# Optimization experiments

Measured on AMD Instinct MI355X. Metric: run time of the kernel, lower is better.

## Reference

```python
import jax, jax.numpy as jnp
from jax import lax
import numpy as np

C_IN, C_OUT, G, K, PAD = 64, 128, 4, 3, 1
P = K * K
CG = C_IN // G
N, H, W = 8, 64, 64
LN_EPS = 1e-6
BN_EPS = 1e-5


def setup_inputs() -> dict:
    key = jax.random.key(0)
    ks = jax.random.split(key, 32)
    r = lambda i, shape, s=0.05: jax.random.normal(ks[i], shape, dtype=jnp.float32) * s
    return dict(
        x=jax.random.normal(ks[0], (N, C_IN, H, W), dtype=jnp.float32),
        reflectance=jax.random.uniform(ks[1], (N, 1, H, W), dtype=jnp.float32),
        gain_w1=r(2, (C_IN, C_IN // 4)), gain_b1=r(3, (C_IN // 4,)),
        gain_w2=r(4, (C_IN // 4, C_IN)), gain_b2=r(5, (C_IN,)),
        tap_w=r(6, (C_IN,)), tap_b=r(7, (C_IN,)),
        dw_w=r(8, (K, K, 1, C_IN)), dw_b=r(9, (C_IN,)),
        ln_g=jnp.ones((C_IN,), jnp.float32), ln_b=jnp.zeros((C_IN,), jnp.float32),
        inp_w=r(10, (C_IN, C_IN)), inp_b=r(11, (C_IN,)),
        off_w=r(12, (C_IN, G * P * 2), 0.02), off_b=r(13, (G * P * 2,), 0.02),
        mask_w=r(14, (C_IN, G * P), 0.02), mask_b=r(15, (G * P,), 0.02),
        outp_w=r(16, (C_IN, C_IN)), outp_b=r(17, (C_IN,)),
        conv_w=r(18, (C_IN, C_OUT)), conv_b=r(19, (C_OUT,)),
        bn1_g=jnp.ones((C_IN,), jnp.float32), bn1_b=jnp.zeros((C_IN,), jnp.float32),
        bn1_m=r(20, (C_IN,)),
        bn1_v=jax.random.uniform(ks[21], (C_IN,), minval=0.5, maxval=1.5),
        bn2_g=jnp.ones((C_OUT,), jnp.float32), bn2_b=jnp.zeros((C_OUT,), jnp.float32),
        bn2_m=r(22, (C_OUT,)),
        bn2_v=jax.random.uniform(ks[23], (C_OUT,), minval=0.5, maxval=1.5),
    )


def _bilinear_gather(xg, py, px):
    # xg: (N, Hp, Wp, G, CG); py/px: (N, H, W, G, P) absolute pixel coords
    # replicates F.grid_sample(mode='bilinear', padding_mode='zeros', align_corners=False)
    n_, Hp, Wp = xg.shape[0], xg.shape[1], xg.shape[2]
    y0 = jnp.floor(py)
    x0 = jnp.floor(px)
    wy = py - y0
    wx = px - x0
    nI = jnp.arange(n_).reshape(n_, 1, 1, 1, 1)
    gI = jnp.arange(G).reshape(1, 1, 1, G, 1)
    out = jnp.zeros(py.shape + (CG,), xg.dtype)
    for dy in (0, 1):
        for dx in (0, 1):
            yi = y0 + dy
            xi = x0 + dx
            w = (wy if dy else 1.0 - wy) * (wx if dx else 1.0 - wx)
            valid = (yi >= 0) & (yi < Hp) & (xi >= 0) & (xi < Wp)
            yc = jnp.clip(yi, 0, Hp - 1).astype(jnp.int32)
            xc = jnp.clip(xi, 0, Wp - 1).astype(jnp.int32)
            v = xg[nI, yc, xc, gI]  # (N, H, W, G, P, CG)
            out = out + (w * valid.astype(w.dtype))[..., None] * v
    return out


def reference(x, reflectance, gain_w1, gain_b1, gain_w2, gain_b2, tap_w, tap_b,
              dw_w, dw_b, ln_g, ln_b, inp_w, inp_b, off_w, off_b, mask_w, mask_b,
              outp_w, outp_b, conv_w, conv_b, bn1_g, bn1_b, bn1_m, bn1_v,
              bn2_g, bn2_b, bn2_m, bn2_v):
    n_, c_, h_, w_ = x.shape
    # ---- GainBlock (SE-style): x * sigmoid(mlp(avgpool(x))) + x ----
    pooled = x.mean(axis=(2, 3))                               # (N, C)
    g = jax.nn.relu(pooled @ gain_w1 + gain_b1)
    gain = jax.nn.sigmoid(g @ gain_w2 + gain_b2)               # (N, C)
    x = x * gain[:, :, None, None] + x
    # ---- ReflectiveFeedback: x + relu(conv1x1(reflectance)) ----
    refl = jax.nn.relu(reflectance * tap_w[None, :, None, None] + tap_b[None, :, None, None])
    x = x + refl                                               # (N, C, H, W)
    # ---- DCNv3 (pytorch version, group=4, k=3, pad=1, stride=1) ----
    xh = jnp.transpose(x, (0, 2, 3, 1))                        # NHWC
    xp = xh @ inp_w + inp_b                                    # input_proj
    dw = lax.conv_general_dilated(xh, dw_w, (1, 1), 'SAME',
                                  feature_group_count=c_,
                                  dimension_numbers=('NHWC', 'HWIO', 'NHWC')) + dw_b
    mu = dw.mean(-1, keepdims=True)
    var = dw.var(-1, keepdims=True)
    dw = ln_g * (dw - mu) * lax.rsqrt(var + LN_EPS) + ln_b     # LN channels_last
    dw = jax.nn.gelu(dw, approximate=False)
    offset = (dw @ off_w + off_b).reshape(n_, h_, w_, G, P, 2)
    mask = jax.nn.softmax((dw @ mask_w + mask_b).reshape(n_, h_, w_, G, P), axis=-1)
    # dcnv3_core: pad input, build reference + dilation grids (normalized by padded size)
    xpad = jnp.pad(xp, ((0, 0), (PAD, PAD), (PAD, PAD), (0, 0)))
    Hp, Wp = h_ + 2 * PAD, w_ + 2 * PAD
    ctr = (K - 1) // 2  # = (dilation*(k-1))//2 with dilation=1
    ref_y = (jnp.arange(h_, dtype=jnp.float32) + ctr + 0.5) / Hp
    ref_x = (jnp.arange(w_, dtype=jnp.float32) + ctr + 0.5) / Wp
    kk = jnp.arange(K, dtype=jnp.float32) - ctr                # [-1, 0, 1]
    gx = jnp.repeat(kk, K) / Wp                                # w-outer, h-inner order
    gy = jnp.tile(kk, K) / Hp
    loc_x = (ref_x[None, None, :, None, None] + gx[None, None, None, None, :]
             + offset[..., 0] / Wp)                            # (N,H,W,G,P)
    loc_y = (ref_y[None, :, None, None, None] + gy[None, None, None, None, :]
             + offset[..., 1] / Hp)
    px = loc_x * Wp - 0.5   # align_corners=False pixel coords
    py = loc_y * Hp - 0.5
    xg = xpad.reshape(n_, Hp, Wp, G, CG)
    samp = _bilinear_gather(xg, py, px)                        # (N,H,W,G,P,CG)
    dcn = (samp * mask[..., None]).sum(axis=4).reshape(n_, h_, w_, c_)
    dcn = dcn @ outp_w + outp_b                                # output_proj
    y = jnp.transpose(dcn, (0, 3, 1, 2))                       # back to NCHW
    # ---- bn1 -> relu -> conv1x1 -> bn2 -> relu (eval-mode BN) ----
    y = bn1_g[None, :, None, None] * (y - bn1_m[None, :, None, None]) \
        * lax.rsqrt(bn1_v[None, :, None, None] + BN_EPS) + bn1_b[None, :, None, None]
    y = jax.nn.relu(y)
    y = jnp.einsum('nchw,cd->ndhw', y, conv_w) + conv_b[None, :, None, None]
    y = bn2_g[None, :, None, None] * (y - bn2_m[None, :, None, None]) \
        * lax.rsqrt(bn2_v[None, :, None, None] + BN_EPS) + bn2_b[None, :, None, None]
    return jax.nn.relu(y)
```

## Files before the change

kernel.cpp:

```cpp
#include <hip/hip_runtime.h>
#include <math.h>


#define WAVE_FENCE() asm volatile("s_waitcnt lgkmcnt(0)" ::: "memory")

__device__ __forceinline__ float2 fma2s(float s, float2 v, float2 acc) {
    acc.x = fmaf(s, v.x, acc.x);
    acc.y = fmaf(s, v.y, acc.y);
    return acc;
}

__global__ __launch_bounds__(256) void k_pool(const float* x, float* pooled) {
    __shared__ float red[256];
    int b = blockIdx.x;
    int nc = ((b & 7) << 6) | (b >> 3);
    const float4* p4 = reinterpret_cast<const float4*>(x + (size_t)nc * 4096);
    float s = 0.f;
    for (int i = threadIdx.x; i < 1024; i += 256) {
        float4 v = p4[i];
        s += v.x + v.y + v.z + v.w;
    }
    red[threadIdx.x] = s;
    __syncthreads();
    for (int o = 128; o > 0; o >>= 1) {
        if (threadIdx.x < o) red[threadIdx.x] += red[threadIdx.x + o];
        __syncthreads();
    }
    if (threadIdx.x == 0) pooled[nc] = red[0] * (1.f / 4096.f);
}

__global__ __launch_bounds__(256) void k_xsproj(
        const float* x, const float* refl,
        const float* tap_w, const float* tap_b,
        const float* pooled,
        const float* gw1, const float* gb1,
        const float* gw2, const float* gb2,
        const float* inp_w, const float* inp_b,
        float* xs, float* xpad) {
    __shared__ float tile[64][65];
    __shared__ float xsw[64][68];
    __shared__ float rr[64];
    __shared__ float gbuf[64];
    int t = threadIdx.x;
    int b = blockIdx.x;
    int n = b & 7, h = b >> 3;
    int c = t & 63, g = t >> 6;

    #pragma unroll
    for (int it = 0; it < 4; ++it) {
        int f = it * 256 + t;
        int cc = f >> 4, w4 = (f & 15) * 4;
        float4 v = *reinterpret_cast<const float4*>(
            &x[(((size_t)(n * 64 + cc)) * 64 + h) * 64 + w4]);
        tile[cc][w4 + 0] = v.x;
        tile[cc][w4 + 1] = v.y;
        tile[cc][w4 + 2] = v.z;
        tile[cc][w4 + 3] = v.w;
    }
    if (t < 64) rr[t] = refl[n * 4096 + h * 64 + t];
    if (t >= 64 && t < 128) {
        int lane = t - 64;
        float pv = pooled[n * 64 + lane];
        float part[16];
        const float4* g4 = reinterpret_cast<const float4*>(gw1 + lane * 16);
        #pragma unroll
        for (int q = 0; q < 4; ++q) {
            float4 v = g4[q];
            part[q * 4 + 0] = pv * v.x;
            part[q * 4 + 1] = pv * v.y;
            part[q * 4 + 2] = pv * v.z;
            part[q * 4 + 3] = pv * v.w;
        }
        #pragma unroll
        for (int o = 32; o > 0; o >>= 1) {
            #pragma unroll
            for (int j = 0; j < 16; ++j) part[j] += __shfl_xor(part[j], o, 64);
        }
        float acc = gb2[lane];
        #pragma unroll
        for (int j = 0; j < 16; ++j) {
            float hj = fmaxf(part[j] + gb1[j], 0.f);
            acc += hj * gw2[j * 64 + lane];
        }
        gbuf[lane] = 1.f + 1.f / (1.f + __expf(-acc));
    }
    __syncthreads();

    {
        float gv = gbuf[c];
        float tw = tap_w[c], tb = tap_b[c];
        float* xsg = xs + (((size_t)(n * 64 + h)) * 64) * 64 + c;
        #pragma unroll
        for (int k = 0; k < 16; ++k) {
            int w = g * 16 + k;
            float r = fmaxf(rr[w] * tw + tb, 0.f);
            float v = tile[c][w] * gv + r;
            xsw[w][c] = v;
            xsg[(size_t)w * 64] = v;
        }
    }
    __syncthreads();

    {
        float acc[16];
        float bv = inp_b[c];
        #pragma unroll
        for (int k = 0; k < 16; ++k) acc[k] = bv;
        for (int c4 = 0; c4 < 64; c4 += 4) {
            float q0 = inp_w[(c4 + 0) * 64 + c];
            float q1 = inp_w[(c4 + 1) * 64 + c];
            float q2 = inp_w[(c4 + 2) * 64 + c];
            float q3 = inp_w[(c4 + 3) * 64 + c];
            #pragma unroll
            for (int k = 0; k < 16; ++k) {
                float4 d = *reinterpret_cast<const float4*>(&xsw[g * 16 + k][c4]);
                acc[k] += d.x * q0 + d.y * q1 + d.z * q2 + d.w * q3;
            }
        }
        const size_t rowb = (((size_t)n * 66) + (h + 1)) * 66;
        #pragma unroll
        for (int k = 0; k < 16; ++k) {
            int w = g * 16 + k;
            xpad[(rowb + (w + 1)) * 64 + c] = acc[k];
        }
        if (g == 0) xpad[rowb * 64 + c] = 0.f;
        if (g == 3) xpad[(rowb + 65) * 64 + c] = 0.f;
        if (h == 0 || h == 63) {
            const size_t base = ((((size_t)n * 66) + (h == 0 ? 0 : 65)) * 66) * 64;
            for (int i = t; i < 66 * 64; i += 256) xpad[base + i] = 0.f;
        }
    }
}

__global__ __launch_bounds__(128, 4) void k_dwsamp(const float* xs, const float* xpad,
                       const float* dw_w, const float* dw_b,
                       const float* ln_g, const float* ln_b,
                       const float* off_w, const float* off_b,
                       const float* mask_w, const float* mask_b,
                       const float* outp_w, const float* outp_b,
                       const float* bn1_g, const float* bn1_b,
                       const float* bn1_m, const float* bn1_v,
                       const float* conv_w, const float* conv_b,
                       const float* bn2_g, const float* bn2_b,
                       const float* bn2_m, const float* bn2_v,
                       float* out) {
    __shared__ float smem[2816];

    int tid = threadIdx.x;
    int lane = tid & 63, wv = tid >> 6;
    float*  chunk = smem + wv * 1408;
    int4*   sad   = reinterpret_cast<int4*>(chunk);
    float*  dwr   = chunk;
    float4* swt   = reinterpret_cast<float4*>(chunk + 576);
    float*  dcnl  = chunk + 1152;
    float*  mlog  = chunk + 1152;

    int b = blockIdx.x;
    int n = b & 7;
    int pos0 = (b >> 3) * 8 + wv * 4;
    int h = pos0 >> 6, w0 = pos0 & 63;

    {
        float dwk[9];
        #pragma unroll
        for (int k = 0; k < 9; ++k) dwk[k] = dw_w[k * 64 + lane];
        float s[4];
        float bvv = dw_b[lane];
        #pragma unroll
        for (int p = 0; p < 4; ++p) s[p] = bvv;
        for (int ky = 0; ky < 3; ++ky) {
            int y = h + ky - 1;
            if (y < 0 || y > 63) continue;
            const float* xrow = xs + ((size_t)(n * 64 + y)) * 4096;
            float v[6];
            #pragma unroll
            for (int dx = 0; dx < 6; ++dx) {
                int x2 = w0 - 1 + dx;
                v[dx] = (x2 >= 0 && x2 <= 63) ? xrow[x2 * 64 + lane] : 0.f;
            }
            float k0 = dwk[ky * 3 + 0], k1 = dwk[ky * 3 + 1], k2 = dwk[ky * 3 + 2];
            #pragma unroll
            for (int p = 0; p < 4; ++p)
                s[p] += v[p] * k0 + v[p + 1] * k1 + v[p + 2] * k2;
        }
        float lngv = ln_g[lane], lnbv = ln_b[lane];
        #pragma unroll
        for (int p = 0; p < 4; ++p) {
            float sv = s[p];
            float sum = sv, sq = sv * sv;
            #pragma unroll
            for (int o = 32; o > 0; o >>= 1) {
                sum += __shfl_xor(sum, o, 64);
                sq  += __shfl_xor(sq,  o, 64);
            }
            float mu = sum * (1.f / 64.f);
            float var = sq * (1.f / 64.f) - mu * mu;
            float nrm = (sv - mu) * rsqrtf(var + 1e-6f) * lngv + lnbv;
            dwr[p * 64 + lane] = 0.5f * nrm * (1.f + erff(nrm * 0.70710678118654752f));
        }
    }
    WAVE_FENCE();

    float2 a01[4];
    {
        int jb = lane * 2;
        const float* wptr;
        int stride;
        float b0 = 0.f, b1 = 0.f;
        if (lane < 36)      { wptr = off_w + jb;         stride = 72; b0 = off_b[jb];       b1 = off_b[jb + 1]; }
        else if (lane < 54) { wptr = mask_w + (jb - 72); stride = 36; b0 = mask_b[jb - 72]; b1 = mask_b[jb - 71]; }
        else                { wptr = off_w;              stride = 0; }
        #pragma unroll
        for (int p = 0; p < 4; ++p) a01[p] = make_float2(b0, b1);
        for (int c4 = 0; c4 < 64; c4 += 4) {
            float4 d0 = *reinterpret_cast<const float4*>(&dwr[0 * 64 + c4]);
            float4 d1 = *reinterpret_cast<const float4*>(&dwr[1 * 64 + c4]);
            float4 d2 = *reinterpret_cast<const float4*>(&dwr[2 * 64 + c4]);
            float4 d3 = *reinterpret_cast<const float4*>(&dwr[3 * 64 + c4]);
            float dk0[4] = {d0.x, d0.y, d0.z, d0.w};
            float dk1[4] = {d1.x, d1.y, d1.z, d1.w};
            float dk2[4] = {d2.x, d2.y, d2.z, d2.w};
            float dk3[4] = {d3.x, d3.y, d3.z, d3.w};
            #pragma unroll
            for (int k = 0; k < 4; ++k) {
                float2 w2 = *reinterpret_cast<const float2*>(wptr);
                wptr += stride;
                a01[0] = fma2s(dk0[k], w2, a01[0]);
                a01[1] = fma2s(dk1[k], w2, a01[1]);
                a01[2] = fma2s(dk2[k], w2, a01[2]);
                a01[3] = fma2s(dk3[k], w2, a01[3]);
            }
        }
        if (lane >= 36 && lane < 54) {
            int jm = lane * 2 - 72;
            #pragma unroll
            for (int p = 0; p < 4; ++p) {
                mlog[p * 40 + jm]     = a01[p].x;
                mlog[p * 40 + jm + 1] = a01[p].y;
            }
        }
    }
    WAVE_FENCE();

    if (lane < 36) {
        int g = lane / 9, pp = lane - g * 9;
        #pragma unroll
        for (int p = 0; p < 4; ++p) {
            const float* lrow = &mlog[p * 40 + g * 9];
            float m = lrow[0];
            #pragma unroll
            for (int k = 1; k < 9; ++k) m = fmaxf(m, lrow[k]);
            float ssum = 0.f, ek = 0.f;
            #pragma unroll
            for (int k = 0; k < 9; ++k) {
                float e = __expf(lrow[k] - m);
                ssum += e;
                if (k == pp) ek = e;
            }
            float mk = ek / ssum;
            float px = (float)((w0 + p) + (pp / 3)) + a01[p].x;
            float py = (float)(h + (pp % 3)) + a01[p].y;
            float x0f = floorf(px), y0f = floorf(py);
            float wx = px - x0f, wy = py - y0f;
            int x0 = (int)x0f, y0 = (int)y0f;
            int x1 = x0 + 1, y1 = y0 + 1;
            int xc0 = min(max(x0, 0), 65), xc1 = min(max(x1, 0), 65);
            int yc0 = min(max(y0, 0), 65), yc1 = min(max(y1, 0), 65);
            float vx0 = (x0 >= 0 && x0 < 66) ? 1.f : 0.f;
            float vx1 = (x1 >= 0 && x1 < 66) ? 1.f : 0.f;
            float vy0 = (y0 >= 0 && y0 < 66) ? 1.f : 0.f;
            float vy1 = (y1 >= 0 && y1 < 66) ? 1.f : 0.f;
            float wx0 = (1.f - wx) * vx0, wx1 = wx * vx1;
            float wy0 = (1.f - wy) * vy0, wy1 = wy * vy1;
            swt[p * 36 + lane] = make_float4(mk * wy0 * wx0, mk * wy0 * wx1,
                                             mk * wy1 * wx0, mk * wy1 * wx1);
            sad[p * 36 + lane] = make_int4((yc0 * 66 + xc0) * 64, (yc0 * 66 + xc1) * 64,
                                           (yc1 * 66 + xc0) * 64, (yc1 * 66 + xc1) * 64);
        }
    }
    WAVE_FENCE();

    {
        int gb = (lane >> 4) * 9;
        const float* xpn = xpad + (size_t)n * 66 * 66 * 64;
        #pragma unroll
        for (int p = 0; p < 4; ++p) {
            float t0[9], t1[9], t2[9], t3[9];
            #pragma unroll
            for (int pp = 0; pp < 9; ++pp) {
                int4 a = sad[p * 36 + gb + pp];
                t0[pp] = xpn[a.x + lane];
                t1[pp] = xpn[a.y + lane];
                t2[pp] = xpn[a.z + lane];
                t3[pp] = xpn[a.w + lane];
            }
            float acc = 0.f;
            #pragma unroll
            for (int pp = 0; pp < 9; ++pp) {
                float4 cw = swt[p * 36 + gb + pp];
                acc += cw.x * t0[pp] + cw.y * t1[pp]
                     + cw.z * t2[pp] + cw.w * t3[pp];
            }
            dcnl[p * 64 + lane] = acc;
        }
    }
    WAVE_FENCE();

    {
        float ob = outp_b[lane];
        float2 s01 = make_float2(ob, ob), s23 = make_float2(ob, ob);
        for (int c4 = 0; c4 < 64; c4 += 4) {
            float w0v = outp_w[(c4 + 0) * 64 + lane];
            float w1v = outp_w[(c4 + 1) * 64 + lane];
            float w2v = outp_w[(c4 + 2) * 64 + lane];
            float w3v = outp_w[(c4 + 3) * 64 + lane];
            float4 d0 = *reinterpret_cast<const float4*>(&dcnl[0 * 64 + c4]);
            float4 d1 = *reinterpret_cast<const float4*>(&dcnl[1 * 64 + c4]);
            float4 d2 = *reinterpret_cast<const float4*>(&dcnl[2 * 64 + c4]);
            float4 d3 = *reinterpret_cast<const float4*>(&dcnl[3 * 64 + c4]);
            s01 = fma2s(w0v, make_float2(d0.x, d1.x), s01);
            s01 = fma2s(w1v, make_float2(d0.y, d1.y), s01);
            s01 = fma2s(w2v, make_float2(d0.z, d1.z), s01);
            s01 = fma2s(w3v, make_float2(d0.w, d1.w), s01);
            s23 = fma2s(w0v, make_float2(d2.x, d3.x), s23);
            s23 = fma2s(w1v, make_float2(d2.y, d3.y), s23);
            s23 = fma2s(w2v, make_float2(d2.z, d3.z), s23);
            s23 = fma2s(w3v, make_float2(d2.w, d3.w), s23);
        }
        float sc = bn1_g[lane] * rsqrtf(bn1_v[lane] + 1e-5f);
        float sh = bn1_b[lane] - sc * bn1_m[lane];
        WAVE_FENCE();
        dcnl[0 * 64 + lane] = fmaxf(sc * s01.x + sh, 0.f);
        dcnl[1 * 64 + lane] = fmaxf(sc * s01.y + sh, 0.f);
        dcnl[2 * 64 + lane] = fmaxf(sc * s23.x + sh, 0.f);
        dcnl[3 * 64 + lane] = fmaxf(sc * s23.y + sh, 0.f);
    }
    WAVE_FENCE();

    {
        float2 acc2[4];
        #pragma unroll
        for (int p = 0; p < 4; ++p) acc2[p] = make_float2(0.f, 0.f);
        for (int c4 = 0; c4 < 64; c4 += 4) {
            float4 d0 = *reinterpret_cast<const float4*>(&dcnl[0 * 64 + c4]);
            float4 d1 = *reinterpret_cast<const float4*>(&dcnl[1 * 64 + c4]);
            float4 d2 = *reinterpret_cast<const float4*>(&dcnl[2 * 64 + c4]);
            float4 d3 = *reinterpret_cast<const float4*>(&dcnl[3 * 64 + c4]);
            float dk0[4] = {d0.x, d0.y, d0.z, d0.w};
            float dk1[4] = {d1.x, d1.y, d1.z, d1.w};
            float dk2[4] = {d2.x, d2.y, d2.z, d2.w};
            float dk3[4] = {d3.x, d3.y, d3.z, d3.w};
            #pragma unroll
            for (int k = 0; k < 4; ++k) {
                float2 w2 = make_float2(conv_w[(c4 + k) * 128 + lane],
                                        conv_w[(c4 + k) * 128 + 64 + lane]);
                acc2[0] = fma2s(dk0[k], w2, acc2[0]);
                acc2[1] = fma2s(dk1[k], w2, acc2[1]);
                acc2[2] = fma2s(dk2[k], w2, acc2[2]);
                acc2[3] = fma2s(dk3[k], w2, acc2[3]);
            }
        }
        int dA = lane, dB = lane + 64;
        float scA = bn2_g[dA] * rsqrtf(bn2_v[dA] + 1e-5f);
        float shA = scA * (conv_b[dA] - bn2_m[dA]) + bn2_b[dA];
        float scB = bn2_g[dB] * rsqrtf(bn2_v[dB] + 1e-5f);
        float shB = scB * (conv_b[dB] - bn2_m[dB]) + bn2_b[dB];
        float4 rA, rB;
        rA.x = fmaxf(scA * acc2[0].x + shA, 0.f);
        rA.y = fmaxf(scA * acc2[1].x + shA, 0.f);
        rA.z = fmaxf(scA * acc2[2].x + shA, 0.f);
        rA.w = fmaxf(scA * acc2[3].x + shA, 0.f);
        rB.x = fmaxf(scB * acc2[0].y + shB, 0.f);
        rB.y = fmaxf(scB * acc2[1].y + shB, 0.f);
        rB.z = fmaxf(scB * acc2[2].y + shB, 0.f);
        rB.w = fmaxf(scB * acc2[3].y + shB, 0.f);
        size_t oA = (((size_t)(n * 128 + dA)) * 64 + h) * 64 + w0;
        size_t oB = (((size_t)(n * 128 + dB)) * 64 + h) * 64 + w0;
        *reinterpret_cast<float4*>(out + oA) = rA;
        *reinterpret_cast<float4*>(out + oB) = rB;
    }
}

extern "C" void kernel_launch(void* const* d_in, const int* in_sizes, int n_in,
                              void* d_out, int out_size, void* d_ws, size_t ws_size,
                              hipStream_t stream) {
    const float* x      = (const float*)d_in[0];
    const float* refl   = (const float*)d_in[1];
    const float* gw1    = (const float*)d_in[2];
    const float* gb1    = (const float*)d_in[3];
    const float* gw2    = (const float*)d_in[4];
    const float* gb2    = (const float*)d_in[5];
    const float* tap_w  = (const float*)d_in[6];
    const float* tap_b  = (const float*)d_in[7];
    const float* dw_w   = (const float*)d_in[8];
    const float* dw_b   = (const float*)d_in[9];
    const float* ln_g   = (const float*)d_in[10];
    const float* ln_b   = (const float*)d_in[11];
    const float* inp_w  = (const float*)d_in[12];
    const float* inp_b  = (const float*)d_in[13];
    const float* off_w  = (const float*)d_in[14];
    const float* off_b  = (const float*)d_in[15];
    const float* mask_w = (const float*)d_in[16];
    const float* mask_b = (const float*)d_in[17];
    const float* outp_w = (const float*)d_in[18];
    const float* outp_b = (const float*)d_in[19];
    const float* conv_w = (const float*)d_in[20];
    const float* conv_b = (const float*)d_in[21];
    const float* bn1_g  = (const float*)d_in[22];
    const float* bn1_b  = (const float*)d_in[23];
    const float* bn1_m  = (const float*)d_in[24];
    const float* bn1_v  = (const float*)d_in[25];
    const float* bn2_g  = (const float*)d_in[26];
    const float* bn2_b  = (const float*)d_in[27];
    const float* bn2_m  = (const float*)d_in[28];
    const float* bn2_v  = (const float*)d_in[29];

    float* ws     = (float*)d_ws;
    float* pooled = ws;
    float* xs     = ws + 512;
    float* xpad   = xs + 2097152;

    k_pool<<<512, 256, 0, stream>>>(x, pooled);
    k_xsproj<<<512, 256, 0, stream>>>(x, refl, tap_w, tap_b, pooled,
                                      gw1, gb1, gw2, gb2,
                                      inp_w, inp_b, xs, xpad);
    k_dwsamp<<<4096, 128, 0, stream>>>(xs, xpad, dw_w, dw_b, ln_g, ln_b,
                                       off_w, off_b, mask_w, mask_b,
                                       outp_w, outp_b, bn1_g, bn1_b, bn1_m, bn1_v,
                                       conv_w, conv_b, bn2_g, bn2_b, bn2_m, bn2_v,
                                       (float*)d_out);
}
```

Baseline: 190.5 us.

## Process eight pixels per wave in fused deformable-conv kernel to reuse weights

Each wave now handles eight output pixels instead of four, doubling the per-wave shared memory chunk and halving the grid. Weight loads for the offset/mask projection, output projection and the 1x1 conv are amortized across twice as many pixels, and the depthwise conv reuses overlapping input columns. The cost is higher register pressure and LDS use per block, which can reduce occupancy under the launch bounds, and fewer blocks to fill the GPU.

```diff
diff --git a/kernel.cpp b/kernel.cpp
--- a/kernel.cpp
+++ b/kernel.cpp
@@ -144,48 +144,48 @@
                        const float* bn2_g, const float* bn2_b,
                        const float* bn2_m, const float* bn2_v,
                        float* out) {
-    __shared__ float smem[2816];
+    __shared__ float smem[5632];
 
     int tid = threadIdx.x;
     int lane = tid & 63, wv = tid >> 6;
-    float*  chunk = smem + wv * 1408;
+    float*  chunk = smem + wv * 2816;
     int4*   sad   = reinterpret_cast<int4*>(chunk);
     float*  dwr   = chunk;
-    float4* swt   = reinterpret_cast<float4*>(chunk + 576);
-    float*  dcnl  = chunk + 1152;
-    float*  mlog  = chunk + 1152;
+    float4* swt   = reinterpret_cast<float4*>(chunk + 1152);
+    float*  dcnl  = chunk + 2304;
+    float*  mlog  = chunk + 2304;
 
     int b = blockIdx.x;
     int n = b & 7;
-    int pos0 = (b >> 3) * 8 + wv * 4;
+    int pos0 = (b >> 3) * 16 + wv * 8;
     int h = pos0 >> 6, w0 = pos0 & 63;
 
     {
         float dwk[9];
         #pragma unroll
         for (int k = 0; k < 9; ++k) dwk[k] = dw_w[k * 64 + lane];
-        float s[4];
+        float s[8];
         float bvv = dw_b[lane];
         #pragma unroll
-        for (int p = 0; p < 4; ++p) s[p] = bvv;
+        for (int p = 0; p < 8; ++p) s[p] = bvv;
         for (int ky = 0; ky < 3; ++ky) {
             int y = h + ky - 1;
             if (y < 0 || y > 63) continue;
             const float* xrow = xs + ((size_t)(n * 64 + y)) * 4096;
-            float v[6];
-            #pragma unroll
-            for (int dx = 0; dx < 6; ++dx) {
+            float v[10];
+            #pragma unroll
+            for (int dx = 0; dx < 10; ++dx) {
                 int x2 = w0 - 1 + dx;
                 v[dx] = (x2 >= 0 && x2 <= 63) ? xrow[x2 * 64 + lane] : 0.f;
             }
             float k0 = dwk[ky * 3 + 0], k1 = dwk[ky * 3 + 1], k2 = dwk[ky * 3 + 2];
             #pragma unroll
-            for (int p = 0; p < 4; ++p)
+            for (int p = 0; p < 8; ++p)
                 s[p] += v[p] * k0 + v[p + 1] * k1 + v[p + 2] * k2;
         }
         float lngv = ln_g[lane], lnbv = ln_b[lane];
         #pragma unroll
-        for (int p = 0; p < 4; ++p) {
+        for (int p = 0; p < 8; ++p) {
             float sv = s[p];
             float sum = sv, sq = sv * sv;
             #pragma unroll
@@ -201,7 +201,7 @@
     }
     WAVE_FENCE();
 
-    float2 a01[4];
+    float2 a01[8];
     {
         int jb = lane * 2;
         const float* wptr;
@@ -211,30 +211,37 @@
         else if (lane < 54) { wptr = mask_w + (jb - 72); stride = 36; b0 = mask_b[jb - 72]; b1 = mask_b[jb - 71]; }
         else                { wptr = off_w;              stride = 0; }
         #pragma unroll
-        for (int p = 0; p < 4; ++p) a01[p] = make_float2(b0, b1);
+        for (int p = 0; p < 8; ++p) a01[p] = make_float2(b0, b1);
         for (int c4 = 0; c4 < 64; c4 += 4) {
-            float4 d0 = *reinterpret_cast<const float4*>(&dwr[0 * 64 + c4]);
-            float4 d1 = *reinterpret_cast<const float4*>(&dwr[1 * 64 + c4]);
-            float4 d2 = *reinterpret_cast<const float4*>(&dwr[2 * 64 + c4]);
-            float4 d3 = *reinterpret_cast<const float4*>(&dwr[3 * 64 + c4]);
-            float dk0[4] = {d0.x, d0.y, d0.z, d0.w};
-            float dk1[4] = {d1.x, d1.y, d1.z, d1.w};
-            float dk2[4] = {d2.x, d2.y, d2.z, d2.w};
-            float dk3[4] = {d3.x, d3.y, d3.z, d3.w};
+            float2 w2a[4];
             #pragma unroll
             for (int k = 0; k < 4; ++k) {
-                float2 w2 = *reinterpret_cast<const float2*>(wptr);
+                w2a[k] = *reinterpret_cast<const float2*>(wptr);
                 wptr += stride;
-                a01[0] = fma2s(dk0[k], w2, a01[0]);
-                a01[1] = fma2s(dk1[k], w2, a01[1]);
-                a01[2] = fma2s(dk2[k], w2, a01[2]);
-                a01[3] = fma2s(dk3[k], w2, a01[3]);
+            }
+            #pragma unroll
+            for (int hf = 0; hf < 2; ++hf) {
+                float4 d0 = *reinterpret_cast<const float4*>(&dwr[(hf * 4 + 0) * 64 + c4]);
+                float4 d1 = *reinterpret_cast<const float4*>(&dwr[(hf * 4 + 1) * 64 + c4]);
+                float4 d2 = *reinterpret_cast<const float4*>(&dwr[(hf * 4 + 2) * 64 + c4]);
+                float4 d3 = *reinterpret_cast<const float4*>(&dwr[(hf * 4 + 3) * 64 + c4]);
+                float dk0[4] = {d0.x, d0.y, d0.z, d0.w};
+                float dk1[4] = {d1.x, d1.y, d1.z, d1.w};
+                float dk2[4] = {d2.x, d2.y, d2.z, d2.w};
+                float dk3[4] = {d3.x, d3.y, d3.z, d3.w};
+                #pragma unroll
+                for (int k = 0; k < 4; ++k) {
+                    a01[hf * 4 + 0] = fma2s(dk0[k], w2a[k], a01[hf * 4 + 0]);
+                    a01[hf * 4 + 1] = fma2s(dk1[k], w2a[k], a01[hf * 4 + 1]);
+                    a01[hf * 4 + 2] = fma2s(dk2[k], w2a[k], a01[hf * 4 + 2]);
+                    a01[hf * 4 + 3] = fma2s(dk3[k], w2a[k], a01[hf * 4 + 3]);
+                }
             }
         }
         if (lane >= 36 && lane < 54) {
             int jm = lane * 2 - 72;
             #pragma unroll
-            for (int p = 0; p < 4; ++p) {
+            for (int p = 0; p < 8; ++p) {
                 mlog[p * 40 + jm]     = a01[p].x;
                 mlog[p * 40 + jm + 1] = a01[p].y;
             }
@@ -245,7 +252,7 @@
     if (lane < 36) {
         int g = lane / 9, pp = lane - g * 9;
         #pragma unroll
-        for (int p = 0; p < 4; ++p) {
+        for (int p = 0; p < 8; ++p) {
             const float* lrow = &mlog[p * 40 + g * 9];
             float m = lrow[0];
             #pragma unroll
@@ -284,7 +291,7 @@
         int gb = (lane >> 4) * 9;
         const float* xpn = xpad + (size_t)n * 66 * 66 * 64;
         #pragma unroll
-        for (int p = 0; p < 4; ++p) {
+        for (int p = 0; p < 8; ++p) {
             float t0[9], t1[9], t2[9], t3[9];
             #pragma unroll
             for (int pp = 0; pp < 9; ++pp) {
@@ -308,56 +315,62 @@
 
     {
         float ob = outp_b[lane];
-        float2 s01 = make_float2(ob, ob), s23 = make_float2(ob, ob);
+        float2 sp[4];
+        #pragma unroll
+        for (int q = 0; q < 4; ++q) sp[q] = make_float2(ob, ob);
         for (int c4 = 0; c4 < 64; c4 += 4) {
             float w0v = outp_w[(c4 + 0) * 64 + lane];
             float w1v = outp_w[(c4 + 1) * 64 + lane];
             float w2v = outp_w[(c4 + 2) * 64 + lane];
             float w3v = outp_w[(c4 + 3) * 64 + lane];
-            float4 d0 = *reinterpret_cast<const float4*>(&dcnl[0 * 64 + c4]);
-            float4 d1 = *reinterpret_cast<const float4*>(&dcnl[1 * 64 + c4]);
-            float4 d2 = *reinterpret_cast<const float4*>(&dcnl[2 * 64 + c4]);
-            float4 d3 = *reinterpret_cast<const float4*>(&dcnl[3 * 64 + c4]);
-            s01 = fma2s(w0v, make_float2(d0.x, d1.x), s01);
-            s01 = fma2s(w1v, make_float2(d0.y, d1.y), s01);
-            s01 = fma2s(w2v, make_float2(d0.z, d1.z), s01);
-            s01 = fma2s(w3v, make_float2(d0.w, d1.w), s01);
-            s23 = fma2s(w0v, make_float2(d2.x, d3.x), s23);
-            s23 = fma2s(w1v, make_float2(d2.y, d3.y), s23);
-            s23 = fma2s(w2v, make_float2(d2.z, d3.z), s23);
-            s23 = fma2s(w3v, make_float2(d2.w, d3.w), s23);
+            #pragma unroll
+            for (int q = 0; q < 4; ++q) {
+                float4 da = *reinterpret_cast<const float4*>(&dcnl[(2 * q + 0) * 64 + c4]);
+                float4 db = *reinterpret_cast<const float4*>(&dcnl[(2 * q + 1) * 64 + c4]);
+                sp[q] = fma2s(w0v, make_float2(da.x, db.x), sp[q]);
+                sp[q] = fma2s(w1v, make_float2(da.y, db.y), sp[q]);
+                sp[q] = fma2s(w2v, make_float2(da.z, db.z), sp[q]);
+                sp[q] = fma2s(w3v, make_float2(da.w, db.w), sp[q]);
+            }
         }
         float sc = bn1_g[lane] * rsqrtf(bn1_v[lane] + 1e-5f);
         float sh = bn1_b[lane] - sc * bn1_m[lane];
         WAVE_FENCE();
-        dcnl[0 * 64 + lane] = fmaxf(sc * s01.x + sh, 0.f);
-        dcnl[1 * 64 + lane] = fmaxf(sc * s01.y + sh, 0.f);
-        dcnl[2 * 64 + lane] = fmaxf(sc * s23.x + sh, 0.f);
-        dcnl[3 * 64 + lane] = fmaxf(sc * s23.y + sh, 0.f);
+        #pragma unroll
+        for (int q = 0; q < 4; ++q) {
+            dcnl[(2 * q + 0) * 64 + lane] = fmaxf(sc * sp[q].x + sh, 0.f);
+            dcnl[(2 * q + 1) * 64 + lane] = fmaxf(sc * sp[q].y + sh, 0.f);
+        }
     }
     WAVE_FENCE();
 
     {
-        float2 acc2[4];
-        #pragma unroll
-        for (int p = 0; p < 4; ++p) acc2[p] = make_float2(0.f, 0.f);
+        float2 acc2[8];
+        #pragma unroll
+        for (int p = 0; p < 8; ++p) acc2[p] = make_float2(0.f, 0.f);
         for (int c4 = 0; c4 < 64; c4 += 4) {
-            float4 d0 = *reinterpret_cast<const float4*>(&dcnl[0 * 64 + c4]);
-            float4 d1 = *reinterpret_cast<const float4*>(&dcnl[1 * 64 + c4]);
-            float4 d2 = *reinterpret_cast<const float4*>(&dcnl[2 * 64 + c4]);
-            float4 d3 = *reinterpret_cast<const float4*>(&dcnl[3 * 64 + c4]);
-            float dk0[4] = {d0.x, d0.y, d0.z, d0.w};
-            float dk1[4] = {d1.x, d1.y, d1.z, d1.w};
-            float dk2[4] = {d2.x, d2.y, d2.z, d2.w};
-            float dk3[4] = {d3.x, d3.y, d3.z, d3.w};
-            #pragma unroll
-            for (int k = 0; k < 4; ++k) {
-                float2 w2 = make_float2(conv_w[(c4 + k) * 128 + lane],
-                                        conv_w[(c4 + k) * 128 + 64 + lane]);
-                acc2[0] = fma2s(dk0[k], w2, acc2[0]);
-                acc2[1] = fma2s(dk1[k], w2, acc2[1]);
-                acc2[2] = fma2s(dk2[k], w2, acc2[2]);
-                acc2[3] = fma2s(dk3[k], w2, acc2[3]);
+            float2 w2a[4];
+            #pragma unroll
+            for (int k = 0; k < 4; ++k)
+                w2a[k] = make_float2(conv_w[(c4 + k) * 128 + lane],
+                                     conv_w[(c4 + k) * 128 + 64 + lane]);
+            #pragma unroll
+            for (int hf = 0; hf < 2; ++hf) {
+                float4 d0 = *reinterpret_cast<const float4*>(&dcnl[(hf * 4 + 0) * 64 + c4]);
+                float4 d1 = *reinterpret_cast<const float4*>(&dcnl[(hf * 4 + 1) * 64 + c4]);
+                float4 d2 = *reinterpret_cast<const float4*>(&dcnl[(hf * 4 + 2) * 64 + c4]);
+                float4 d3 = *reinterpret_cast<const float4*>(&dcnl[(hf * 4 + 3) * 64 + c4]);
+                float dk0[4] = {d0.x, d0.y, d0.z, d0.w};
+                float dk1[4] = {d1.x, d1.y, d1.z, d1.w};
+                float dk2[4] = {d2.x, d2.y, d2.z, d2.w};
+                float dk3[4] = {d3.x, d3.y, d3.z, d3.w};
+                #pragma unroll
+                for (int k = 0; k < 4; ++k) {
+                    acc2[hf * 4 + 0] = fma2s(dk0[k], w2a[k], acc2[hf * 4 + 0]);
+                    acc2[hf * 4 + 1] = fma2s(dk1[k], w2a[k], acc2[hf * 4 + 1]);
+                    acc2[hf * 4 + 2] = fma2s(dk2[k], w2a[k], acc2[hf * 4 + 2]);
+                    acc2[hf * 4 + 3] = fma2s(dk3[k], w2a[k], acc2[hf * 4 + 3]);
+                }
             }
         }
         int dA = lane, dB = lane + 64;
@@ -365,19 +378,22 @@
         float shA = scA * (conv_b[dA] - bn2_m[dA]) + bn2_b[dA];
         float scB = bn2_g[dB] * rsqrtf(bn2_v[dB] + 1e-5f);
         float shB = scB * (conv_b[dB] - bn2_m[dB]) + bn2_b[dB];
-        float4 rA, rB;
-        rA.x = fmaxf(scA * acc2[0].x + shA, 0.f);
-        rA.y = fmaxf(scA * acc2[1].x + shA, 0.f);
-        rA.z = fmaxf(scA * acc2[2].x + shA, 0.f);
-        rA.w = fmaxf(scA * acc2[3].x + shA, 0.f);
-        rB.x = fmaxf(scB * acc2[0].y + shB, 0.f);
-        rB.y = fmaxf(scB * acc2[1].y + shB, 0.f);
-        rB.z = fmaxf(scB * acc2[2].y + shB, 0.f);
-        rB.w = fmaxf(scB * acc2[3].y + shB, 0.f);
         size_t oA = (((size_t)(n * 128 + dA)) * 64 + h) * 64 + w0;
         size_t oB = (((size_t)(n * 128 + dB)) * 64 + h) * 64 + w0;
-        *reinterpret_cast<float4*>(out + oA) = rA;
-        *reinterpret_cast<float4*>(out + oB) = rB;
+        #pragma unroll
+        for (int hf = 0; hf < 2; ++hf) {
+            float4 rA, rB;
+            rA.x = fmaxf(scA * acc2[hf * 4 + 0].x + shA, 0.f);
+            rA.y = fmaxf(scA * acc2[hf * 4 + 1].x + shA, 0.f);
+            rA.z = fmaxf(scA * acc2[hf * 4 + 2].x + shA, 0.f);
+            rA.w = fmaxf(scA * acc2[hf * 4 + 3].x + shA, 0.f);
+            rB.x = fmaxf(scB * acc2[hf * 4 + 0].y + shB, 0.f);
+            rB.y = fmaxf(scB * acc2[hf * 4 + 1].y + shB, 0.f);
+            rB.z = fmaxf(scB * acc2[hf * 4 + 2].y + shB, 0.f);
+            rB.w = fmaxf(scB * acc2[hf * 4 + 3].y + shB, 0.f);
+            *reinterpret_cast<float4*>(out + oA + hf * 4) = rA;
+            *reinterpret_cast<float4*>(out + oB + hf * 4) = rB;
+        }
     }
 }
 
@@ -424,7 +440,7 @@
     k_xsproj<<<512, 256, 0, stream>>>(x, refl, tap_w, tap_b, pooled,
                                       gw1, gb1, gw2, gb2,
                                       inp_w, inp_b, xs, xpad);
-    k_dwsamp<<<4096, 128, 0, stream>>>(xs, xpad, dw_w, dw_b, ln_g, ln_b,
+    k_dwsamp<<<2048, 128, 0, stream>>>(xs, xpad, dw_w, dw_b, ln_g, ln_b,
                                        off_w, off_b, mask_w, mask_b,
                                        outp_w, outp_b, bn1_g, bn1_b, bn1_m, bn1_v,
                                        conv_w, conv_b, bn2_g, bn2_b, bn2_m, bn2_v,
```

New measurement: 205.6 us. 8.0% more time.

## Fuse global pooling into projection kernel via per-batch atomic grid sync

Applied to the files above, without the earlier changes.

Removes the separate pooling kernel, which read all of x a second time. Each block of the projection kernel now writes per-row channel partial sums, and the last block to finish for each batch (found with an atomic counter) computes the gain MLP and sets a flag. All blocks of that batch spin on the flag before applying the gain. This saves one full pass over x and one launch, but it adds a memset and relies on every block of a batch being resident at once, which risks deadlock or stalls if they are not.

```diff
diff --git a/kernel.cpp b/kernel.cpp
--- a/kernel.cpp
+++ b/kernel.cpp
@@ -10,41 +10,24 @@
     return acc;
 }
 
-__global__ __launch_bounds__(256) void k_pool(const float* x, float* pooled) {
-    __shared__ float red[256];
-    int b = blockIdx.x;
-    int nc = ((b & 7) << 6) | (b >> 3);
-    const float4* p4 = reinterpret_cast<const float4*>(x + (size_t)nc * 4096);
-    float s = 0.f;
-    for (int i = threadIdx.x; i < 1024; i += 256) {
-        float4 v = p4[i];
-        s += v.x + v.y + v.z + v.w;
-    }
-    red[threadIdx.x] = s;
-    __syncthreads();
-    for (int o = 128; o > 0; o >>= 1) {
-        if (threadIdx.x < o) red[threadIdx.x] += red[threadIdx.x + o];
-        __syncthreads();
-    }
-    if (threadIdx.x == 0) pooled[nc] = red[0] * (1.f / 4096.f);
-}
-
-__global__ __launch_bounds__(256) void k_xsproj(
+__global__ __launch_bounds__(256) void k_pre(
         const float* x, const float* refl,
         const float* tap_w, const float* tap_b,
-        const float* pooled,
         const float* gw1, const float* gb1,
         const float* gw2, const float* gb2,
         const float* inp_w, const float* inp_b,
+        int* sync, float* gaing, float* parts,
         float* xs, float* xpad) {
     __shared__ float tile[64][65];
     __shared__ float xsw[64][68];
     __shared__ float rr[64];
-    __shared__ float gbuf[64];
+    __shared__ int comp;
     int t = threadIdx.x;
     int b = blockIdx.x;
     int n = b & 7, h = b >> 3;
     int c = t & 63, g = t >> 6;
+    int* cnt  = sync;
+    int* flag = sync + 8;
 
     #pragma unroll
     for (int it = 0; it < 4; ++it) {
@@ -58,36 +41,76 @@
         tile[cc][w4 + 3] = v.w;
     }
     if (t < 64) rr[t] = refl[n * 4096 + h * 64 + t];
-    if (t >= 64 && t < 128) {
-        int lane = t - 64;
-        float pv = pooled[n * 64 + lane];
-        float part[16];
-        const float4* g4 = reinterpret_cast<const float4*>(gw1 + lane * 16);
-        #pragma unroll
-        for (int q = 0; q < 4; ++q) {
-            float4 v = g4[q];
-            part[q * 4 + 0] = pv * v.x;
-            part[q * 4 + 1] = pv * v.y;
-            part[q * 4 + 2] = pv * v.z;
-            part[q * 4 + 3] = pv * v.w;
-        }
-        #pragma unroll
-        for (int o = 32; o > 0; o >>= 1) {
-            #pragma unroll
-            for (int j = 0; j < 16; ++j) part[j] += __shfl_xor(part[j], o, 64);
-        }
-        float acc = gb2[lane];
-        #pragma unroll
-        for (int j = 0; j < 16; ++j) {
-            float hj = fmaxf(part[j] + gb1[j], 0.f);
-            acc += hj * gw2[j * 64 + lane];
-        }
-        gbuf[lane] = 1.f + 1.f / (1.f + __expf(-acc));
-    }
-    __syncthreads();
-
-    {
-        float gv = gbuf[c];
+    __syncthreads();
+
+    {
+        float rs = 0.f;
+        #pragma unroll
+        for (int k = 0; k < 16; ++k) rs += tile[c][g * 16 + k];
+        xsw[g][c] = rs;
+    }
+    __syncthreads();
+    if (t < 64) {
+        float tot = xsw[0][t] + xsw[1][t] + xsw[2][t] + xsw[3][t];
+        parts[((size_t)(n * 64 + h)) * 64 + t] = tot;
+    }
+    __syncthreads();
+    if (t == 0) {
+        __threadfence();
+        int old = __hip_atomic_fetch_add(&cnt[n], 1, __ATOMIC_ACQ_REL,
+                                         __HIP_MEMORY_SCOPE_AGENT);
+        comp = (old == 63) ? 1 : 0;
+    }
+    __syncthreads();
+
+    if (comp) {
+        if (t < 64) {
+            __builtin_amdgcn_fence(__ATOMIC_ACQUIRE, "agent");
+            int lane = t;
+            float pv = 0.f;
+            for (int hh = 0; hh < 64; ++hh)
+                pv += parts[((size_t)(n * 64 + hh)) * 64 + lane];
+            pv *= (1.f / 4096.f);
+            float part[16];
+            const float4* g4 = reinterpret_cast<const float4*>(gw1 + lane * 16);
+            #pragma unroll
+            for (int q = 0; q < 4; ++q) {
+                float4 v = g4[q];
+                part[q * 4 + 0] = pv * v.x;
+                part[q * 4 + 1] = pv * v.y;
+                part[q * 4 + 2] = pv * v.z;
+                part[q * 4 + 3] = pv * v.w;
+            }
+            #pragma unroll
+            for (int o = 32; o > 0; o >>= 1) {
+                #pragma unroll
+                for (int j = 0; j < 16; ++j) part[j] += __shfl_xor(part[j], o, 64);
+            }
+            float acc = gb2[lane];
+            #pragma unroll
+            for (int j = 0; j < 16; ++j) {
+                float hj = fmaxf(part[j] + gb1[j], 0.f);
+                acc += hj * gw2[j * 64 + lane];
+            }
+            gaing[n * 64 + lane] = 1.f + 1.f / (1.f + __expf(-acc));
+        }
+        __syncthreads();
+        if (t == 0) {
+            __threadfence();
+            __hip_atomic_store(&flag[n], 1, __ATOMIC_RELEASE,
+                               __HIP_MEMORY_SCOPE_AGENT);
+        }
+    }
+    if (t == 0) {
+        while (__hip_atomic_load(&flag[n], __ATOMIC_RELAXED,
+                                 __HIP_MEMORY_SCOPE_AGENT) == 0)
+            __builtin_amdgcn_s_sleep(16);
+        __builtin_amdgcn_fence(__ATOMIC_ACQUIRE, "agent");
+    }
+    __syncthreads();
+
+    {
+        float gv = gaing[n * 64 + c];
         float tw = tap_w[c], tb = tap_b[c];
         float* xsg = xs + (((size_t)(n * 64 + h)) * 64) * 64 + c;
         #pragma unroll
@@ -416,14 +439,16 @@
     const float* bn2_v  = (const float*)d_in[29];
 
     float* ws     = (float*)d_ws;
-    float* pooled = ws;
-    float* xs     = ws + 512;
+    int*   sync   = (int*)ws;
+    float* gaing  = ws + 16;
+    float* parts  = ws + 528;
+    float* xs     = ws + 33296;
     float* xpad   = xs + 2097152;
 
-    k_pool<<<512, 256, 0, stream>>>(x, pooled);
-    k_xsproj<<<512, 256, 0, stream>>>(x, refl, tap_w, tap_b, pooled,
-                                      gw1, gb1, gw2, gb2,
-                                      inp_w, inp_b, xs, xpad);
+    hipMemsetAsync(sync, 0, 16 * sizeof(int), stream);
+    k_pre<<<512, 256, 0, stream>>>(x, refl, tap_w, tap_b,
+                                   gw1, gb1, gw2, gb2, inp_w, inp_b,
+                                   sync, gaing, parts, xs, xpad);
     k_dwsamp<<<4096, 128, 0, stream>>>(xs, xpad, dw_w, dw_b, ln_g, ln_b,
                                        off_w, off_b, mask_w, mask_b,
                                        outp_w, outp_b, bn1_g, bn1_b, bn1_m, bn1_v,
```

New measurement: 212.1 us. +11.3%, slower.

## Store padded features as horizontal pixel pairs for float2 bilinear gathers

Applied to the files above, without the earlier changes.

The producer kernel now writes each padded pixel's channels interleaved with its right neighbour's (pair layout, 128 floats per position). The sampler can then fetch both horizontal bilinear corners with one float2 load, halving the gather instructions and the address table in shared memory. Edge handling remaps the x weights onto the left and right slots of the clamped base. This doubles the xpad workspace and the write traffic in the producer, and it relies on the workspace being large enough.

```diff
diff --git a/kernel.cpp b/kernel.cpp
--- a/kernel.cpp
+++ b/kernel.cpp
@@ -7,6 +7,11 @@
 __device__ __forceinline__ float2 fma2s(float s, float2 v, float2 acc) {
     acc.x = fmaf(s, v.x, acc.x);
     acc.y = fmaf(s, v.y, acc.y);
+    return acc;
+}
+__device__ __forceinline__ float2 fma22(float2 a, float2 v, float2 acc) {
+    acc.x = fmaf(a.x, v.x, acc.x);
+    acc.y = fmaf(a.y, v.y, acc.y);
     return acc;
 }
 
@@ -36,7 +41,7 @@
         const float* gw1, const float* gb1,
         const float* gw2, const float* gb2,
         const float* inp_w, const float* inp_b,
-        float* xs, float* xpad) {
+        float* xs, float* xpad2) {
     __shared__ float tile[64][65];
     __shared__ float xsw[64][68];
     __shared__ float rr[64];
@@ -120,19 +125,21 @@
         const size_t rowb = (((size_t)n * 66) + (h + 1)) * 66;
         #pragma unroll
         for (int k = 0; k < 16; ++k) {
-            int w = g * 16 + k;
-            xpad[(rowb + (w + 1)) * 64 + c] = acc[k];
-        }
-        if (g == 0) xpad[rowb * 64 + c] = 0.f;
-        if (g == 3) xpad[(rowb + 65) * 64 + c] = 0.f;
+            int xx = g * 16 + k + 1;
+            float v = acc[k];
+            xpad2[(rowb + xx) * 128 + c * 2 + 0]     = v;
+            xpad2[(rowb + xx - 1) * 128 + c * 2 + 1] = v;
+        }
+        if (g == 0) xpad2[rowb * 128 + c * 2 + 0] = 0.f;
+        if (g == 3) xpad2[(rowb + 64) * 128 + c * 2 + 1] = 0.f;
         if (h == 0 || h == 63) {
-            const size_t base = ((((size_t)n * 66) + (h == 0 ? 0 : 65)) * 66) * 64;
-            for (int i = t; i < 66 * 64; i += 256) xpad[base + i] = 0.f;
-        }
-    }
-}
-
-__global__ __launch_bounds__(128, 4) void k_dwsamp(const float* xs, const float* xpad,
+            const size_t base = ((((size_t)n * 66) + (h == 0 ? 0 : 65)) * 66) * 128;
+            for (int i = t; i < 66 * 128; i += 256) xpad2[base + i] = 0.f;
+        }
+    }
+}
+
+__global__ __launch_bounds__(128, 4) void k_dwsamp(const float* xs, const float* xpad2,
                        const float* dw_w, const float* dw_b,
                        const float* ln_g, const float* ln_b,
                        const float* off_w, const float* off_b,
@@ -144,16 +151,16 @@
                        const float* bn2_g, const float* bn2_b,
                        const float* bn2_m, const float* bn2_v,
                        float* out) {
-    __shared__ float smem[2816];
+    __shared__ float smem[2240];
 
     int tid = threadIdx.x;
     int lane = tid & 63, wv = tid >> 6;
-    float*  chunk = smem + wv * 1408;
-    int4*   sad   = reinterpret_cast<int4*>(chunk);
+    float*  chunk = smem + wv * 1120;
+    int2*   sad2  = reinterpret_cast<int2*>(chunk);
     float*  dwr   = chunk;
-    float4* swt   = reinterpret_cast<float4*>(chunk + 576);
-    float*  dcnl  = chunk + 1152;
-    float*  mlog  = chunk + 1152;
+    float4* swt   = reinterpret_cast<float4*>(chunk + 288);
+    float*  dcnl  = chunk + 864;
+    float*  mlog  = chunk + 864;
 
     int b = blockIdx.x;
     int n = b & 7;
@@ -264,44 +271,45 @@
             float wx = px - x0f, wy = py - y0f;
             int x0 = (int)x0f, y0 = (int)y0f;
             int x1 = x0 + 1, y1 = y0 + 1;
-            int xc0 = min(max(x0, 0), 65), xc1 = min(max(x1, 0), 65);
             int yc0 = min(max(y0, 0), 65), yc1 = min(max(y1, 0), 65);
-            float vx0 = (x0 >= 0 && x0 < 66) ? 1.f : 0.f;
-            float vx1 = (x1 >= 0 && x1 < 66) ? 1.f : 0.f;
             float vy0 = (y0 >= 0 && y0 < 66) ? 1.f : 0.f;
             float vy1 = (y1 >= 0 && y1 < 66) ? 1.f : 0.f;
-            float wx0 = (1.f - wx) * vx0, wx1 = wx * vx1;
-            float wy0 = (1.f - wy) * vy0, wy1 = wy * vy1;
-            swt[p * 36 + lane] = make_float4(mk * wy0 * wx0, mk * wy0 * wx1,
-                                             mk * wy1 * wx0, mk * wy1 * wx1);
-            sad[p * 36 + lane] = make_int4((yc0 * 66 + xc0) * 64, (yc0 * 66 + xc1) * 64,
-                                           (yc1 * 66 + xc0) * 64, (yc1 * 66 + xc1) * 64);
+            int xc0 = min(max(x0, 0), 65), xc1 = min(max(x1, 0), 65);
+            float wx0 = ((x0 >= 0 && x0 < 66) ? 1.f : 0.f) * (1.f - wx);
+            float wx1 = ((x1 >= 0 && x1 < 66) ? 1.f : 0.f) * wx;
+            int xb = min(max(x0, 0), 64);
+            float wl = (xc0 == xb     ? wx0 : 0.f) + (xc1 == xb     ? wx1 : 0.f);
+            float wr = (xc0 == xb + 1 ? wx0 : 0.f) + (xc1 == xb + 1 ? wx1 : 0.f);
+            float wy0m = mk * ((1.f - wy) * vy0);
+            float wy1m = mk * (wy * vy1);
+            swt[p * 36 + lane]  = make_float4(wy0m * wl, wy0m * wr,
+                                              wy1m * wl, wy1m * wr);
+            sad2[p * 36 + lane] = make_int2((yc0 * 66 + xb) * 128,
+                                            (yc1 * 66 + xb) * 128);
         }
     }
     WAVE_FENCE();
 
     {
         int gb = (lane >> 4) * 9;
-        const float* xpn = xpad + (size_t)n * 66 * 66 * 64;
+        const float* xpn = xpad2 + (size_t)n * 66 * 66 * 128;
         #pragma unroll
         for (int p = 0; p < 4; ++p) {
-            float t0[9], t1[9], t2[9], t3[9];
+            float2 t0[9], t1[9];
             #pragma unroll
             for (int pp = 0; pp < 9; ++pp) {
-                int4 a = sad[p * 36 + gb + pp];
-                t0[pp] = xpn[a.x + lane];
-                t1[pp] = xpn[a.y + lane];
-                t2[pp] = xpn[a.z + lane];
-                t3[pp] = xpn[a.w + lane];
-            }
-            float acc = 0.f;
+                int2 a = sad2[p * 36 + gb + pp];
+                t0[pp] = *reinterpret_cast<const float2*>(xpn + a.x + lane * 2);
+                t1[pp] = *reinterpret_cast<const float2*>(xpn + a.y + lane * 2);
+            }
+            float2 acc2 = make_float2(0.f, 0.f);
             #pragma unroll
             for (int pp = 0; pp < 9; ++pp) {
                 float4 cw = swt[p * 36 + gb + pp];
-                acc += cw.x * t0[pp] + cw.y * t1[pp]
-                     + cw.z * t2[pp] + cw.w * t3[pp];
-            }
-            dcnl[p * 64 + lane] = acc;
+                acc2 = fma22(make_float2(cw.x, cw.y), t0[pp], acc2);
+                acc2 = fma22(make_float2(cw.z, cw.w), t1[pp], acc2);
+            }
+            dcnl[p * 64 + lane] = acc2.x + acc2.y;
         }
     }
     WAVE_FENCE();
@@ -418,13 +426,13 @@
     float* ws     = (float*)d_ws;
     float* pooled = ws;
     float* xs     = ws + 512;
-    float* xpad   = xs + 2097152;
+    float* xpad2  = xs + 2097152;
 
     k_pool<<<512, 256, 0, stream>>>(x, pooled);
     k_xsproj<<<512, 256, 0, stream>>>(x, refl, tap_w, tap_b, pooled,
                                       gw1, gb1, gw2, gb2,
-                                      inp_w, inp_b, xs, xpad);
-    k_dwsamp<<<4096, 128, 0, stream>>>(xs, xpad, dw_w, dw_b, ln_g, ln_b,
+                                      inp_w, inp_b, xs, xpad2);
+    k_dwsamp<<<4096, 128, 0, stream>>>(xs, xpad2, dw_w, dw_b, ln_g, ln_b,
                                        off_w, off_b, mask_w, mask_b,
                                        outp_w, outp_b, bn1_g, bn1_b, bn1_m, bn1_v,
                                        conv_w, conv_b, bn2_g, bn2_b, bn2_m, bn2_v,
```

Result: slower. 202.2 us (+6.2%).
